# Kernel tuning notes

Hardware: AMD Instinct MI355X
Metric: run time of the kernel (lower is better)

## Reference

```python
import jax, jax.numpy as jnp
import numpy as np

B, N, C, OUT = 1, 16384, 32, 256


def _he(k, fan_in, shape):
    return jax.random.normal(k, shape, jnp.float32) * np.sqrt(2.0 / fan_in).astype(np.float32)


def setup_inputs() -> dict:
    key = jax.random.key(0)
    ks = jax.random.split(key, 16)
    x = jax.random.normal(ks[0], (B, N, C), jnp.float32)
    adjacency = jax.random.uniform(ks[1], (B, N, N), jnp.float32)
    # global_mlp: C -> 1024 -> 1024 -> OUT (ReLU after every linear)
    g_w1 = _he(ks[2], C, (C, 1024)); g_b1 = jnp.zeros((1024,), jnp.float32)
    g_w2 = _he(ks[3], 1024, (1024, 1024)); g_b2 = jnp.zeros((1024,), jnp.float32)
    g_w3 = _he(ks[4], 1024, (1024, OUT)); g_b3 = jnp.zeros((OUT,), jnp.float32)
    # attention_mlp: C -> 128 -> 64 -> 1 (ReLU after first two linears)
    a_w1 = _he(ks[5], C, (C, 128)); a_b1 = jnp.zeros((128,), jnp.float32)
    a_w2 = _he(ks[6], 128, (128, 64)); a_b2 = jnp.zeros((64,), jnp.float32)
    a_w3 = _he(ks[7], 64, (64, 1)); a_b3 = jnp.zeros((1,), jnp.float32)
    return dict(x=x, adjacency=adjacency,
                g_w1=g_w1, g_b1=g_b1, g_w2=g_w2, g_b2=g_b2, g_w3=g_w3, g_b3=g_b3,
                a_w1=a_w1, a_b1=a_b1, a_w2=a_w2, a_b2=a_b2, a_w3=a_w3, a_b3=a_b3)


def _global_mlp(h, w1, b1, w2, b2, w3, b3):
    h = jax.nn.relu(h @ w1 + b1)
    h = jax.nn.relu(h @ w2 + b2)
    return jax.nn.relu(h @ w3 + b3)


def reference(x, adjacency, g_w1, g_b1, g_w2, g_b2, g_w3, g_b3,
              a_w1, a_b1, a_w2, a_b2, a_w3, a_b3):
    # attention scores per node: [B, N]
    h = jax.nn.relu(x @ a_w1 + a_b1)
    h = jax.nn.relu(h @ a_w2 + a_b2)
    scores = (h @ a_w3 + a_b3)[..., 0]
    attn = jax.nn.softmax(scores, axis=1)[..., None]            # [B, N, 1]
    wf = x * attn                                               # [B, N, C]
    gc = wf.sum(axis=1)                                         # [B, C]
    out = _global_mlp(gc, g_w1, g_b1, g_w2, g_b2, g_w3, g_b3)   # [B, OUT]
    # diagonal of (A @ WF) @ WF^T without materializing [B,N,N]:
    aw = jnp.matmul(adjacency, wf)                              # [B, N, C]
    diag = (aw * wf).sum(axis=-1)                               # [B, N]
    context_signal = diag.mean(axis=1)                          # [B]
    # torch broadcast [B,C] + [B] is only valid for B==1; same here.
    gc2 = gc + 0.001 * context_signal
    for _ in range(2):
        out = out + 0.001 * _global_mlp(gc2, g_w1, g_b1, g_w2, g_b2, g_w3, g_b3)
    return out
```

## Files before the change

kernel.cpp:

```cpp
#include <hip/hip_runtime.h>
#include <hip/hip_bf16.h>
#include <math.h>

#define N_NODES 16384
#define C_IN 32

typedef __attribute__((ext_vector_type(8))) short short8;
typedef __attribute__((ext_vector_type(4))) short s16x4;
typedef __attribute__((ext_vector_type(4))) float f32x4;
typedef __attribute__((ext_vector_type(4))) float f4v;

__device__ __forceinline__ unsigned short f2bf(float f) {
    unsigned u = __float_as_uint(f);
    u = u + 0x7fffu + ((u >> 16) & 1u);
    return (unsigned short)(u >> 16);
}

__global__ void k_zero(float* __restrict__ p) {
    p[threadIdx.x] = 0.f;
}

__global__ __launch_bounds__(256) void k_attn_scores(
    const float* __restrict__ x,
    const float* __restrict__ aw1, const float* __restrict__ ab1,
    const float* __restrict__ aw2, const float* __restrict__ ab2,
    const float* __restrict__ aw3, const float* __restrict__ ab3,
    float* __restrict__ scores)
{
    __shared__ float w1s[4096];
    __shared__ float w2s[8192];
    __shared__ float b1s[128];
    __shared__ float b2s[64];
    __shared__ float w3s[64];
    __shared__ float xs[256];
    __shared__ float h1s[1024];

    const int tid = threadIdx.x;
    for (int i = tid; i < 4096; i += 256) w1s[i] = aw1[i];
    for (int i = tid; i < 8192; i += 256) w2s[i] = aw2[i];
    if (tid < 128) b1s[tid] = ab1[tid];
    if (tid < 64)  { b2s[tid] = ab2[tid]; w3s[tid] = aw3[tid]; }
    xs[tid] = x[(size_t)blockIdx.x * 256 + tid];
    __syncthreads();

    const int nl  = tid >> 5;
    const int t31 = tid & 31;

    float a0 = b1s[t31*4+0], a1 = b1s[t31*4+1], a2 = b1s[t31*4+2], a3 = b1s[t31*4+3];
    #pragma unroll
    for (int c = 0; c < 32; ++c) {
        float xv = xs[nl*32 + c];
        float4 w = *(const float4*)&w1s[c*128 + t31*4];
        a0 += xv * w.x; a1 += xv * w.y; a2 += xv * w.z; a3 += xv * w.w;
    }
    *(float4*)&h1s[nl*128 + t31*4] =
        make_float4(fmaxf(a0,0.f), fmaxf(a1,0.f), fmaxf(a2,0.f), fmaxf(a3,0.f));
    __syncthreads();

    float c0 = b2s[t31*2], c1 = b2s[t31*2 + 1];
    #pragma unroll 8
    for (int o = 0; o < 128; ++o) {
        float hv = h1s[nl*128 + o];
        float2 w = *(const float2*)&w2s[o*64 + t31*2];
        c0 += hv * w.x;
        c1 += hv * w.y;
    }
    float s = fmaxf(c0, 0.f) * w3s[t31*2] + fmaxf(c1, 0.f) * w3s[t31*2 + 1];
    s += __shfl_xor(s, 1);  s += __shfl_xor(s, 2);  s += __shfl_xor(s, 4);
    s += __shfl_xor(s, 8);  s += __shfl_xor(s, 16);
    if (t31 == 0) scores[(size_t)blockIdx.x * 8 + nl] = s + ab3[0];
}

__global__ __launch_bounds__(1024) void k_softmax_red(
    const float* __restrict__ scores, float* __restrict__ red)
{
    __shared__ float sm[1024];
    const int tid = threadIdx.x;
    float m = -3.4e38f;
    for (int i = tid; i < N_NODES; i += 1024) m = fmaxf(m, scores[i]);
    sm[tid] = m; __syncthreads();
    for (int s = 512; s > 0; s >>= 1) {
        if (tid < s) sm[tid] = fmaxf(sm[tid], sm[tid + s]);
        __syncthreads();
    }
    m = sm[0];
    __syncthreads();
    float acc = 0.f;
    for (int i = tid; i < N_NODES; i += 1024) acc += expf(scores[i] - m);
    sm[tid] = acc; __syncthreads();
    for (int s = 512; s > 0; s >>= 1) {
        if (tid < s) sm[tid] += sm[tid + s];
        __syncthreads();
    }
    if (tid == 0) { red[0] = m; red[1] = sm[0]; }
}

__global__ __launch_bounds__(256) void k_attn_wf(
    const float* __restrict__ scores, const float* __restrict__ red,
    const float* __restrict__ x, float* __restrict__ attn,
    unsigned short* __restrict__ wfT, float* __restrict__ gc)
{
    const int n = blockIdx.x * 256 + threadIdx.x;
    const float m = red[0], s = red[1];
    const float a = expf(scores[n] - m) / s;
    attn[n] = a;

    float wv[32];
    const float4* xr = (const float4*)(x + (size_t)n * 32);
    #pragma unroll
    for (int q = 0; q < 8; ++q) {
        float4 v = xr[q];
        wv[q*4+0] = v.x * a; wv[q*4+1] = v.y * a;
        wv[q*4+2] = v.z * a; wv[q*4+3] = v.w * a;
    }
    #pragma unroll
    for (int c = 0; c < 32; ++c)
        wfT[(size_t)c * N_NODES + n] = f2bf(wv[c]);

    const int lane = threadIdx.x & 63;
    #pragma unroll
    for (int c = 0; c < 32; ++c) {
        float v = wv[c];
        v += __shfl_xor(v, 1);  v += __shfl_xor(v, 2);  v += __shfl_xor(v, 4);
        v += __shfl_xor(v, 8);  v += __shfl_xor(v, 16); v += __shfl_xor(v, 32);
        if (lane == 0) atomicAdd(&gc[c], v);
    }
}

__device__ __forceinline__ void a_issue(const float* __restrict__ A,
    int i0, int gcol, int lane, f4v (&dst)[4])
{
    const int rlo = lane >> 4, c16 = (lane & 15) * 4;
    #pragma unroll
    for (int r = 0; r < 4; ++r)
        dst[r] = __builtin_nontemporal_load(
            (const f4v*)(A + (size_t)(i0 + 4*r + rlo) * N_NODES + gcol + c16));
}

__device__ __forceinline__ void a_write(char* wb, int lane, const f4v (&src)[4])
{
    const int rlo = lane >> 4, cb = (lane & 15) * 8;
    #pragma unroll
    for (int r = 0; r < 4; ++r) {
        const int row = 4*r + rlo;
        s16x4 w;
        w[0] = (short)f2bf(src[r][0]); w[1] = (short)f2bf(src[r][1]);
        w[2] = (short)f2bf(src[r][2]); w[3] = (short)f2bf(src[r][3]);
        *(s16x4*)(wb + row*128 + (cb ^ ((row & 7) << 4))) = w;
    }
}

template<int T>
__device__ __forceinline__ void ctx_step(
    const float* __restrict__ A, const unsigned short* __restrict__ sB_u,
    char* wbase, int i0, int gcol0, int lane, int q, int r16,
    f4v (&iss)[4], f4v (&wr)[4], f32x4& acc0, f32x4& acc1)
{
    const char* sBb = (const char*)sB_u;
    const int swz = (r16 & 7) << 4;
    short8 b00 = *(const short8*)(sBb + r16*1024      + ((T*128      + q*16) ^ swz));
    short8 b01 = *(const short8*)(sBb + r16*1024      + ((T*128 + 64 + q*16) ^ swz));
    short8 b10 = *(const short8*)(sBb + (r16+16)*1024 + ((T*128      + q*16) ^ swz));
    short8 b11 = *(const short8*)(sBb + (r16+16)*1024 + ((T*128 + 64 + q*16) ^ swz));
    if constexpr (T + 4 < 8)
        a_issue(A, i0, gcol0 + (T + 4) * 64, lane, iss);
    const char* ab = wbase + (T & 1) * 2048;
    short8 av0 = *(const short8*)(ab + r16*128 + ((     q*16) ^ swz));
    short8 av1 = *(const short8*)(ab + r16*128 + ((64 + q*16) ^ swz));
    acc0 = __builtin_amdgcn_mfma_f32_16x16x32_bf16(av0, b00, acc0, 0, 0, 0);
    acc1 = __builtin_amdgcn_mfma_f32_16x16x32_bf16(av0, b10, acc1, 0, 0, 0);
    acc0 = __builtin_amdgcn_mfma_f32_16x16x32_bf16(av1, b01, acc0, 0, 0, 0);
    acc1 = __builtin_amdgcn_mfma_f32_16x16x32_bf16(av1, b11, acc1, 0, 0, 0);
    if constexpr (T + 1 < 8)
        a_write(wbase + ((T + 1) & 1) * 2048, lane, wr);
    __builtin_amdgcn_sched_barrier(0);
}

__global__ __launch_bounds__(256, 3) void k_context(
    const float* __restrict__ A, const unsigned short* __restrict__ wfT,
    const float* __restrict__ x, const float* __restrict__ attn,
    float* __restrict__ partials)
{
    __shared__ unsigned short sB_u[32 * 512];
    __shared__ short sA[4][2][1024];
    __shared__ float sRed[4];

    const int tid  = threadIdx.x;
    const int wid  = tid >> 6, lane = tid & 63;
    const int rb   = blockIdx.x & 255;
    const int js   = blockIdx.x >> 8;
    const int i0   = rb * 64 + wid * 16;
    const int gcol0 = js * 512;

    const int q   = lane >> 4;
    const int r16 = lane & 15;
    char* wbase = (char*)sA[wid];

    f32x4 acc0 = {0.f, 0.f, 0.f, 0.f};
    f32x4 acc1 = {0.f, 0.f, 0.f, 0.f};

    f4v s0[4], s1[4], s2[4], s3[4];

    a_issue(A, i0, gcol0,       lane, s0);
    a_issue(A, i0, gcol0 + 64,  lane, s1);
    a_issue(A, i0, gcol0 + 128, lane, s2);
    a_issue(A, i0, gcol0 + 192, lane, s3);

    {
        const int row = tid >> 3;
        const unsigned short* gB = wfT + (size_t)row * N_NODES + gcol0;
        char* lB = (char*)sB_u + row * 1024;
        #pragma unroll
        for (int c = 0; c < 8; ++c) {
            const int chunk = (tid & 7) + 8 * c;
            short8 v = *(const short8*)(gB + chunk * 8);
            *(short8*)(lB + ((chunk * 16) ^ ((row & 7) << 4))) = v;
        }
    }
    __syncthreads();
    a_write(wbase, lane, s0);
    __builtin_amdgcn_sched_barrier(0);

    ctx_step<0>(A, sB_u, wbase, i0, gcol0, lane, q, r16, s0, s1, acc0, acc1);
    ctx_step<1>(A, sB_u, wbase, i0, gcol0, lane, q, r16, s1, s2, acc0, acc1);
    ctx_step<2>(A, sB_u, wbase, i0, gcol0, lane, q, r16, s2, s3, acc0, acc1);
    ctx_step<3>(A, sB_u, wbase, i0, gcol0, lane, q, r16, s3, s0, acc0, acc1);
    ctx_step<4>(A, sB_u, wbase, i0, gcol0, lane, q, r16, s0, s1, acc0, acc1);
    ctx_step<5>(A, sB_u, wbase, i0, gcol0, lane, q, r16, s1, s2, acc0, acc1);
    ctx_step<6>(A, sB_u, wbase, i0, gcol0, lane, q, r16, s2, s3, acc0, acc1);
    ctx_step<7>(A, sB_u, wbase, i0, gcol0, lane, q, r16, s3, s0, acc0, acc1);

    float partial = 0.f;
    #pragma unroll
    for (int r = 0; r < 4; ++r) {
        const int i = i0 + q * 4 + r;
        const float a = attn[i];
        partial += acc0[r] * (x[(size_t)i * 32 + r16]      * a);
        partial += acc1[r] * (x[(size_t)i * 32 + 16 + r16] * a);
    }
    partial += __shfl_xor(partial, 1);  partial += __shfl_xor(partial, 2);
    partial += __shfl_xor(partial, 4);  partial += __shfl_xor(partial, 8);
    partial += __shfl_xor(partial, 16); partial += __shfl_xor(partial, 32);
    if (lane == 0) sRed[wid] = partial;
    __syncthreads();
    if (tid == 0) partials[blockIdx.x] = (sRed[0] + sRed[1]) + (sRed[2] + sRed[3]);
}

__global__ __launch_bounds__(1024) void k_mlp1(
    const float* __restrict__ gc, const float* __restrict__ partials,
    const float* __restrict__ w1, const float* __restrict__ b1,
    float* __restrict__ h1ab)
{
    __shared__ float sm[1024];
    __shared__ float g1[32], g2[32];
    const int t = threadIdx.x;
    float acc = 0.f;
    #pragma unroll
    for (int i = 0; i < 8; ++i) acc += partials[t + 1024 * i];
    sm[t] = acc; __syncthreads();
    for (int s = 512; s > 0; s >>= 1) {
        if (t < s) sm[t] += sm[t + s];
        __syncthreads();
    }
    if (t < 32) {
        float cs = sm[0] * (1.0f / 16384.0f);
        g1[t] = gc[t];
        g2[t] = gc[t] + 0.001f * cs;
    }
    __syncthreads();
    float s1 = b1[t], s2 = b1[t];
    #pragma unroll
    for (int c = 0; c < 32; ++c) {
        float wv = w1[(size_t)c * 1024 + t];
        s1 += g1[c] * wv;
        s2 += g2[c] * wv;
    }
    h1ab[t]        = fmaxf(s1, 0.f);
    h1ab[1024 + t] = fmaxf(s2, 0.f);
}

__global__ __launch_bounds__(256) void k_mlp2(
    const float* __restrict__ h1ab, const float* __restrict__ w2,
    const float* __restrict__ b2, float* __restrict__ h2ab)
{
    __shared__ float h1s[1024];
    __shared__ float sm[256];
    const int v   = blockIdx.x & 1;
    const int ob  = blockIdx.x >> 1;
    const int tid = threadIdx.x;
    const int o   = tid & 15, g = tid >> 4;
    for (int i = tid; i < 1024; i += 256) h1s[i] = h1ab[v * 1024 + i];
    __syncthreads();
    const float* wp = w2 + (size_t)(g * 64) * 1024 + ob * 16 + o;
    float acc = 0.f;
    #pragma unroll 8
    for (int k = 0; k < 64; ++k)
        acc += h1s[g * 64 + k] * wp[(size_t)k * 1024];
    sm[tid] = acc;
    __syncthreads();
    if (tid < 16) {
        float s = b2[ob * 16 + tid];
        #pragma unroll
        for (int g2 = 0; g2 < 16; ++g2) s += sm[g2 * 16 + tid];
        h2ab[v * 1024 + ob * 16 + tid] = fmaxf(s, 0.f);
    }
}

__global__ __launch_bounds__(512) void k_mlp3(
    const float* __restrict__ h2ab, const float* __restrict__ w3,
    const float* __restrict__ b3, float* __restrict__ out)
{
    __shared__ float sm[512];
    const int tid = threadIdx.x;
    const int v   = tid >> 8;
    const int g   = (tid >> 4) & 15;
    const int o   = tid & 15;
    const int ob  = blockIdx.x;
    const float* hp = h2ab + v * 1024 + g * 64;
    const float* wp = w3 + (size_t)(g * 64) * 256 + ob * 16 + o;
    float acc = 0.f;
    #pragma unroll 8
    for (int k = 0; k < 64; ++k)
        acc += hp[k] * wp[(size_t)k * 256];
    sm[tid] = acc;
    __syncthreads();
    if (tid < 16) {
        float pa = b3[ob * 16 + tid], pb = pa;
        #pragma unroll
        for (int g2 = 0; g2 < 16; ++g2) {
            pa += sm[g2 * 16 + tid];
            pb += sm[256 + g2 * 16 + tid];
        }
        out[ob * 16 + tid] = fmaxf(pa, 0.f) + 0.002f * fmaxf(pb, 0.f);
    }
}

extern "C" void kernel_launch(void* const* d_in, const int* in_sizes, int n_in,
                              void* d_out, int out_size, void* d_ws, size_t ws_size,
                              hipStream_t stream)
{
    const float* x   = (const float*)d_in[0];
    const float* A   = (const float*)d_in[1];
    const float* gw1 = (const float*)d_in[2];
    const float* gb1 = (const float*)d_in[3];
    const float* gw2 = (const float*)d_in[4];
    const float* gb2 = (const float*)d_in[5];
    const float* gw3 = (const float*)d_in[6];
    const float* gb3 = (const float*)d_in[7];
    const float* aw1 = (const float*)d_in[8];
    const float* ab1 = (const float*)d_in[9];
    const float* aw2 = (const float*)d_in[10];
    const float* ab2 = (const float*)d_in[11];
    const float* aw3 = (const float*)d_in[12];
    const float* ab3 = (const float*)d_in[13];
    float* out = (float*)d_out;

    char* ws = (char*)d_ws;
    float* scores   = (float*)(ws + 0);
    float* attn     = (float*)(ws + 65536);
    float* red      = (float*)(ws + 131072);
    float* gc       = (float*)(ws + 131328);
    float* h1ab     = (float*)(ws + 131584);
    float* h2ab     = (float*)(ws + 139776);
    float* partials = (float*)(ws + 163840);
    unsigned short* wfT = (unsigned short*)(ws + 262144);

    k_zero       <<<1,    32,   0, stream>>>(gc);
    k_attn_scores<<<N_NODES/8, 256, 0, stream>>>(x, aw1, ab1, aw2, ab2, aw3, ab3, scores);
    k_softmax_red<<<1,    1024, 0, stream>>>(scores, red);
    k_attn_wf    <<<N_NODES/256, 256, 0, stream>>>(scores, red, x, attn, wfT, gc);
    k_context    <<<8192, 256,  0, stream>>>(A, wfT, x, attn, partials);
    k_mlp1       <<<1,    1024, 0, stream>>>(gc, partials, gw1, gb1, h1ab);
    k_mlp2       <<<128,  256,  0, stream>>>(h1ab, gw2, gb2, h2ab);
    k_mlp3       <<<16,   512,  0, stream>>>(h2ab, gw3, gb3, out);
}
```

Measured before the change: 304.9 us.

## Halve context column tile and load whole A tile up front instead of software pipeline

The adjacency-times-weighted-features kernel now gives each block 256 columns instead of 512 and doubles the grid to 16384 blocks. Each wave issues all 16 rows of its A tile at once into registers, converts them to bf16 into a single swizzled LDS buffer, then runs 8 MFMA k-steps. This replaces the previous double-buffered, four-deep prefetch pipeline. The goal is simpler code with more memory-level parallelism per wave, at the cost of losing overlap between loads and compute inside a block, more registers, and twice as many partials for the reduction.

```diff
diff --git a/kernel.cpp b/kernel.cpp
--- a/kernel.cpp
+++ b/kernel.cpp
@@ -127,108 +127,66 @@
     }
 }
 
-__device__ __forceinline__ void a_issue(const float* __restrict__ A,
-    int i0, int gcol, int lane, f4v (&dst)[4])
-{
-    const int rlo = lane >> 4, c16 = (lane & 15) * 4;
-    #pragma unroll
-    for (int r = 0; r < 4; ++r)
-        dst[r] = __builtin_nontemporal_load(
-            (const f4v*)(A + (size_t)(i0 + 4*r + rlo) * N_NODES + gcol + c16));
-}
-
-__device__ __forceinline__ void a_write(char* wb, int lane, const f4v (&src)[4])
-{
-    const int rlo = lane >> 4, cb = (lane & 15) * 8;
-    #pragma unroll
-    for (int r = 0; r < 4; ++r) {
-        const int row = 4*r + rlo;
-        s16x4 w;
-        w[0] = (short)f2bf(src[r][0]); w[1] = (short)f2bf(src[r][1]);
-        w[2] = (short)f2bf(src[r][2]); w[3] = (short)f2bf(src[r][3]);
-        *(s16x4*)(wb + row*128 + (cb ^ ((row & 7) << 4))) = w;
-    }
-}
-
-template<int T>
-__device__ __forceinline__ void ctx_step(
-    const float* __restrict__ A, const unsigned short* __restrict__ sB_u,
-    char* wbase, int i0, int gcol0, int lane, int q, int r16,
-    f4v (&iss)[4], f4v (&wr)[4], f32x4& acc0, f32x4& acc1)
-{
-    const char* sBb = (const char*)sB_u;
-    const int swz = (r16 & 7) << 4;
-    short8 b00 = *(const short8*)(sBb + r16*1024      + ((T*128      + q*16) ^ swz));
-    short8 b01 = *(const short8*)(sBb + r16*1024      + ((T*128 + 64 + q*16) ^ swz));
-    short8 b10 = *(const short8*)(sBb + (r16+16)*1024 + ((T*128      + q*16) ^ swz));
-    short8 b11 = *(const short8*)(sBb + (r16+16)*1024 + ((T*128 + 64 + q*16) ^ swz));
-    if constexpr (T + 4 < 8)
-        a_issue(A, i0, gcol0 + (T + 4) * 64, lane, iss);
-    const char* ab = wbase + (T & 1) * 2048;
-    short8 av0 = *(const short8*)(ab + r16*128 + ((     q*16) ^ swz));
-    short8 av1 = *(const short8*)(ab + r16*128 + ((64 + q*16) ^ swz));
-    acc0 = __builtin_amdgcn_mfma_f32_16x16x32_bf16(av0, b00, acc0, 0, 0, 0);
-    acc1 = __builtin_amdgcn_mfma_f32_16x16x32_bf16(av0, b10, acc1, 0, 0, 0);
-    acc0 = __builtin_amdgcn_mfma_f32_16x16x32_bf16(av1, b01, acc0, 0, 0, 0);
-    acc1 = __builtin_amdgcn_mfma_f32_16x16x32_bf16(av1, b11, acc1, 0, 0, 0);
-    if constexpr (T + 1 < 8)
-        a_write(wbase + ((T + 1) & 1) * 2048, lane, wr);
-    __builtin_amdgcn_sched_barrier(0);
-}
-
 __global__ __launch_bounds__(256, 3) void k_context(
     const float* __restrict__ A, const unsigned short* __restrict__ wfT,
     const float* __restrict__ x, const float* __restrict__ attn,
     float* __restrict__ partials)
 {
-    __shared__ unsigned short sB_u[32 * 512];
-    __shared__ short sA[4][2][1024];
+    __shared__ unsigned short sB_u[32 * 256];
+    __shared__ short sA[4][16 * 256];
     __shared__ float sRed[4];
 
-    const int tid  = threadIdx.x;
-    const int wid  = tid >> 6, lane = tid & 63;
-    const int rb   = blockIdx.x & 255;
-    const int js   = blockIdx.x >> 8;
-    const int i0   = rb * 64 + wid * 16;
-    const int gcol0 = js * 512;
+    const int tid   = threadIdx.x;
+    const int wid   = tid >> 6, lane = tid & 63;
+    const int rb    = blockIdx.x & 255;
+    const int js    = blockIdx.x >> 8;
+    const int i0    = rb * 64 + wid * 16;
+    const int gcol0 = js * 256;
 
     const int q   = lane >> 4;
     const int r16 = lane & 15;
     char* wbase = (char*)sA[wid];
 
-    f32x4 acc0 = {0.f, 0.f, 0.f, 0.f};
-    f32x4 acc1 = {0.f, 0.f, 0.f, 0.f};
-
-    f4v s0[4], s1[4], s2[4], s3[4];
-
-    a_issue(A, i0, gcol0,       lane, s0);
-    a_issue(A, i0, gcol0 + 64,  lane, s1);
-    a_issue(A, i0, gcol0 + 128, lane, s2);
-    a_issue(A, i0, gcol0 + 192, lane, s3);
+    f4v av[16];
+    #pragma unroll
+    for (int r = 0; r < 16; ++r)
+        av[r] = __builtin_nontemporal_load(
+            (const f4v*)(A + (size_t)(i0 + r) * N_NODES + gcol0 + lane * 4));
 
     {
         const int row = tid >> 3;
         const unsigned short* gB = wfT + (size_t)row * N_NODES + gcol0;
-        char* lB = (char*)sB_u + row * 1024;
+        char* lB = (char*)sB_u + row * 512;
         #pragma unroll
-        for (int c = 0; c < 8; ++c) {
+        for (int c = 0; c < 4; ++c) {
             const int chunk = (tid & 7) + 8 * c;
             short8 v = *(const short8*)(gB + chunk * 8);
             *(short8*)(lB + ((chunk * 16) ^ ((row & 7) << 4))) = v;
         }
     }
     __syncthreads();
-    a_write(wbase, lane, s0);
-    __builtin_amdgcn_sched_barrier(0);
-
-    ctx_step<0>(A, sB_u, wbase, i0, gcol0, lane, q, r16, s0, s1, acc0, acc1);
-    ctx_step<1>(A, sB_u, wbase, i0, gcol0, lane, q, r16, s1, s2, acc0, acc1);
-    ctx_step<2>(A, sB_u, wbase, i0, gcol0, lane, q, r16, s2, s3, acc0, acc1);
-    ctx_step<3>(A, sB_u, wbase, i0, gcol0, lane, q, r16, s3, s0, acc0, acc1);
-    ctx_step<4>(A, sB_u, wbase, i0, gcol0, lane, q, r16, s0, s1, acc0, acc1);
-    ctx_step<5>(A, sB_u, wbase, i0, gcol0, lane, q, r16, s1, s2, acc0, acc1);
-    ctx_step<6>(A, sB_u, wbase, i0, gcol0, lane, q, r16, s2, s3, acc0, acc1);
-    ctx_step<7>(A, sB_u, wbase, i0, gcol0, lane, q, r16, s3, s0, acc0, acc1);
+
+    #pragma unroll
+    for (int r = 0; r < 16; ++r) {
+        s16x4 w;
+        w[0] = (short)f2bf(av[r][0]); w[1] = (short)f2bf(av[r][1]);
+        w[2] = (short)f2bf(av[r][2]); w[3] = (short)f2bf(av[r][3]);
+        *(s16x4*)(wbase + r * 512 + ((lane * 8) ^ ((r & 7) << 4))) = w;
+    }
+
+    f32x4 acc0 = {0.f, 0.f, 0.f, 0.f};
+    f32x4 acc1 = {0.f, 0.f, 0.f, 0.f};
+    const int swzA = (r16 & 7) << 4;
+    const char* sBb = (const char*)sB_u;
+    #pragma unroll
+    for (int kk = 0; kk < 8; ++kk) {
+        const int fo = kk * 64 + q * 16;
+        short8 afr = *(const short8*)(wbase + r16 * 512 + (fo ^ swzA));
+        short8 b0  = *(const short8*)(sBb + r16 * 512        + (fo ^ swzA));
+        short8 b1  = *(const short8*)(sBb + (r16 + 16) * 512 + (fo ^ swzA));
+        acc0 = __builtin_amdgcn_mfma_f32_16x16x32_bf16(afr, b0, acc0, 0, 0, 0);
+        acc1 = __builtin_amdgcn_mfma_f32_16x16x32_bf16(afr, b1, acc1, 0, 0, 0);
+    }
 
     float partial = 0.f;
     #pragma unroll
@@ -256,7 +214,7 @@
     const int t = threadIdx.x;
     float acc = 0.f;
     #pragma unroll
-    for (int i = 0; i < 8; ++i) acc += partials[t + 1024 * i];
+    for (int i = 0; i < 16; ++i) acc += partials[t + 1024 * i];
     sm[t] = acc; __syncthreads();
     for (int s = 512; s > 0; s >>= 1) {
         if (t < s) sm[t] += sm[t + s];
@@ -369,7 +327,7 @@
     k_attn_scores<<<N_NODES/8, 256, 0, stream>>>(x, aw1, ab1, aw2, ab2, aw3, ab3, scores);
     k_softmax_red<<<1,    1024, 0, stream>>>(scores, red);
     k_attn_wf    <<<N_NODES/256, 256, 0, stream>>>(scores, red, x, attn, wfT, gc);
-    k_context    <<<8192, 256,  0, stream>>>(A, wfT, x, attn, partials);
+    k_context    <<<16384, 256, 0, stream>>>(A, wfT, x, attn, partials);
     k_mlp1       <<<1,    1024, 0, stream>>>(gc, partials, gw1, gb1, h1ab);
     k_mlp2       <<<128,  256,  0, stream>>>(h1ab, gw2, gb2, h2ab);
     k_mlp3       <<<16,   512,  0, stream>>>(h2ab, gw3, gb3, out);
```

Result: faster. 295.8 us (-3.0%).
